# Kernel tuning notes

Measured on AMD Instinct MI355X. Metric: run time of the kernel, lower is better.

The kernel has to match this reference:

```python
import jax, jax.numpy as jnp
import numpy as np

SCALING_FACTOR = 128.0


def setup_inputs() -> dict:
    key = jax.random.key(0)
    k1, k2, k3, k4 = jax.random.split(key, 4)
    B, G1, G2, DX, DZ, NT = 4, 128, 128, 2, 128, 2048
    x_grid = jax.random.uniform(k1, (B, G1, G2, DX), dtype=jnp.float32)
    z_grid = jax.random.normal(k2, (B, G1, G2, DZ), dtype=jnp.float32)
    xt = jax.random.uniform(k3, (B, NT, DX), dtype=jnp.float32)
    # raw (pre-softplus) lengthscale parameter, one per input dim
    init_ls = 0.1
    lengthscale_param = jnp.full((DX,), np.log(np.exp(init_ls) - 1.0), dtype=jnp.float32)
    lengthscale_param = lengthscale_param + 0.01 * jax.random.normal(k4, (DX,), dtype=jnp.float32)
    return {"x_grid": x_grid, "z_grid": z_grid, "xt": xt, "lengthscale_param": lengthscale_param}


def reference(x_grid, z_grid, xt, lengthscale_param):
    B = x_grid.shape[0]
    dx = x_grid.shape[-1]
    dz = z_grid.shape[-1]
    # flatten spatial grid dims -> (B, ng, d)
    xg = x_grid.reshape(B, -1, dx)
    zg = z_grid.reshape(B, -1, dz)
    # lengthscale = 1e-5 + softplus(param), shape (dx,)
    ls = 1e-5 + jax.nn.softplus(lengthscale_param)
    # pairwise scaled squared distances: (B, nt, ng)
    diff = (xt[:, :, None, :] - xg[:, None, :, :]) / ls  # (B, nt, ng, dx)
    dist2 = jnp.sum(diff * diff, axis=-1)
    weights = jnp.exp(-0.5 * dist2)  # (B, nt, ng)
    # weighted smoothing onto targets
    out = jnp.einsum("btg,bgz->btz", weights, zg) / SCALING_FACTOR
    return out
```

## Files before the change

### kernel.cpp

```cpp
#include <hip/hip_runtime.h>
#include <hip/hip_bf16.h>
#include <cstdint>
#include <cstddef>


typedef float  f32x4  __attribute__((ext_vector_type(4)));
typedef float  f32x16 __attribute__((ext_vector_type(16)));
typedef short  short8 __attribute__((ext_vector_type(8)));
typedef unsigned short ushort8 __attribute__((ext_vector_type(8)));

#if __has_builtin(__builtin_amdgcn_exp2f)
#define EXP2F(x) __builtin_amdgcn_exp2f(x)
#else
#define EXP2F(x) exp2f(x)
#endif

#define AS1C(p) ((const __attribute__((address_space(1))) void*)(p))
#define AS3(p)  ((__attribute__((address_space(3))) void*)(p))

__device__ __forceinline__ unsigned short bf16_bits(float f) {
  __bf16 h = (__bf16)f;
  return __builtin_bit_cast(unsigned short, h);
}

__global__ __launch_bounds__(256) void pre_kernel(
    const float* __restrict__ x_grid, const float* __restrict__ z_grid,
    const float* __restrict__ xt, const float* __restrict__ lsp,
    unsigned short* __restrict__ zgb, float* __restrict__ xg_trip,
    float* __restrict__ xt_trip)
{
  const int bid = blockIdx.x;
  const int b   = bid >> 9;
  const int t   = bid & 511;
  const int tid = threadIdx.x;

  const size_t zbase = (size_t)b * 16384 * 128;
  unsigned short* dst_tile = zgb + ((size_t)(b * 512 + t)) * 4096;

  #pragma unroll
  for (int it = 0; it < 2; ++it) {
    const int o8 = it * 256 + tid;
    const int h  = o8 >> 8;
    const int q2 = (o8 >> 7) & 1;
    const int c  = o8 & 127;
    const int kb = t * 32 + h * 16 + q2 * 4;
    ushort8 v;
    #pragma unroll
    for (int hi = 0; hi < 2; ++hi)
      #pragma unroll
      for (int j = 0; j < 4; ++j) {
        float f = z_grid[zbase + (size_t)(kb + 8 * hi + j) * 128 + c];
        v[hi * 4 + j] = bf16_bits(f);
      }
    *(ushort8*)(dst_tile + o8 * 8) = v;
  }

  if (tid < 64) {
    const float ls0 = 1e-5f + log1pf(expf(lsp[0]));
    const float ls1 = 1e-5f + log1pf(expf(lsp[1]));
    const float cs  = sqrtf(0.7213475204444817f);
    const float s0 = cs / ls0, s1 = cs / ls1;
    if (tid < 32) {
      const int g = t * 32 + tid;
      const float u0 = x_grid[(size_t)(b * 16384 + g) * 2 + 0] * s0;
      const float u1 = x_grid[(size_t)(b * 16384 + g) * 2 + 1] * s1;
      float* d = xg_trip + (size_t)(b * 512 + t) * 96 + tid * 3;
      d[0] = 2.0f * u0; d[1] = 2.0f * u1; d[2] = -(u0 * u0 + u1 * u1);
    } else if (t < 64) {
      const int r = t * 32 + (tid - 32);
      const float u0 = xt[(size_t)(b * 2048 + r) * 2 + 0] * s0;
      const float u1 = xt[(size_t)(b * 2048 + r) * 2 + 1] * s1;
      float* d = xt_trip + (size_t)(b * 2048 + r) * 3;
      d[0] = u0; d[1] = u1; d[2] = -(u0 * u0 + u1 * u1);
    }
  }
}

__global__ __launch_bounds__(512, 2) void main_kernel(
    const unsigned short* __restrict__ zgb,
    const float* __restrict__ xg_trip,
    const float* __restrict__ xt_trip,
    float* __restrict__ partials)
{
  __shared__ __align__(128) char smem[24576];
  char*  zbuf  = smem;
  float* xgbuf = (float*)(smem + 16384);

  const int bid = blockIdx.x;
  const int ks  = bid & 3;
  const int mt  = (bid >> 2) & 15;
  const int b   = bid >> 6;

  const int tid = threadIdx.x;
  const int wv  = tid >> 6;
  const int l   = tid & 63;
  const int rh  = wv & 1;
  const int kp  = wv >> 1;
  const int h   = kp & 1;
  const int tp  = kp >> 1;
  const int l31 = l & 31;
  const int q2  = l >> 5;

  float at0[2], at1[2], ca[2];
  #pragma unroll
  for (int mi = 0; mi < 2; ++mi) {
    const int r = mt * 128 + rh * 64 + mi * 32 + l31;
    const float* p = xt_trip + (size_t)(b * 2048 + r) * 3;
    at0[mi] = p[0]; at1[mi] = p[1]; ca[mi] = p[2];
  }

  f32x16 acc[2][4];
  #pragma unroll
  for (int mi = 0; mi < 2; ++mi)
    #pragma unroll
    for (int ni = 0; ni < 4; ++ni)
      #pragma unroll
      for (int e = 0; e < 16; ++e)
        acc[mi][ni][e] = 0.0f;

  const size_t tilebase = (size_t)(b * 512 + ks * 128);
  const char*  zsrc = (const char*)zgb + tilebase * 8192;
  const char*  xsrc = (const char*)(xg_trip) + tilebase * 384;

  auto stage = [&](int t, int bb) {
    __builtin_amdgcn_global_load_lds(
        AS1C(zsrc + (size_t)t * 8192 + wv * 1024 + l * 16),
        AS3(zbuf + bb * 8192 + wv * 1024 + l * 16), 16, 0, 0);
    if (l < 3) {
      __builtin_amdgcn_global_load_lds(
          AS1C(xsrc + (size_t)t * 384 + wv * 48 + l * 16),
          AS3((char*)xgbuf + bb * 384 + wv * 48 + l * 16), 16, 0, 0);
    }
  };

  stage(0, 0);

  for (int t = 0; t < 128; ++t) {
    __syncthreads();
    if (t + 1 < 128) stage(t + 1, (t + 1) & 1);
    if ((t & 1) == tp) {
      const int bb = t & 1;

      const f32x4* xq = (const f32x4*)(xgbuf + bb * 96 + (h * 16 + q2 * 4) * 3);
      const f32x4 A0 = xq[0], A1 = xq[1], A2 = xq[2];
      const f32x4 B0 = xq[6], B1 = xq[7], B2 = xq[8];
      float g0[8], g1[8], cb[8];
      g0[0]=A0.x; g1[0]=A0.y; cb[0]=A0.z;
      g0[1]=A0.w; g1[1]=A1.x; cb[1]=A1.y;
      g0[2]=A1.z; g1[2]=A1.w; cb[2]=A2.x;
      g0[3]=A2.y; g1[3]=A2.z; cb[3]=A2.w;
      g0[4]=B0.x; g1[4]=B0.y; cb[4]=B0.z;
      g0[5]=B0.w; g1[5]=B1.x; cb[5]=B1.y;
      g0[6]=B1.z; g1[6]=B1.w; cb[6]=B2.x;
      g0[7]=B2.y; g1[7]=B2.z; cb[7]=B2.w;

      short8 af[2];
      #pragma unroll
      for (int mi = 0; mi < 2; ++mi) {
        union { short8 s; __bf16 e[8]; } u;
        #pragma unroll
        for (int j = 0; j < 8; ++j) {
          float arg = __builtin_fmaf(at0[mi], g0[j],
                      __builtin_fmaf(at1[mi], g1[j], ca[mi] + cb[j]));
          u.e[j] = (__bf16)EXP2F(arg);
        }
        af[mi] = u.s;
      }

      const char* zt = zbuf + bb * 8192 + h * 4096 + (q2 * 128 + l31) * 16;
      short8 bfr[4];
      #pragma unroll
      for (int ni = 0; ni < 4; ++ni)
        bfr[ni] = *(const short8*)(zt + ni * 512);

      #pragma unroll
      for (int mi = 0; mi < 2; ++mi)
        #pragma unroll
        for (int ni = 0; ni < 4; ++ni)
          acc[mi][ni] = __builtin_amdgcn_mfma_f32_32x32x16_bf16(
              af[mi], bfr[ni], acc[mi][ni], 0, 0, 0);
    }
  }

  __syncthreads();
  float* red = (float*)smem;
  float* pb = partials + ((size_t)(ks * 64 + b * 16 + mt)) * 16384;

  #pragma unroll
  for (int mi = 0; mi < 2; ++mi)
    #pragma unroll
    for (int ni = 0; ni < 4; ++ni) {
      if (kp != 0)
        *(f32x16*)(red + ((rh * 3 + (kp - 1)) * 64 + l) * 16) = acc[mi][ni];
      __syncthreads();
      if (kp == 0) {
        f32x16 s = acc[mi][ni];
        #pragma unroll
        for (int src = 0; src < 3; ++src) {
          const f32x4* sp = (const f32x4*)(red + ((rh * 3 + src) * 64 + l) * 16);
          #pragma unroll
          for (int q = 0; q < 4; ++q) {
            f32x4 v = sp[q];
            s[q*4+0] += v.x; s[q*4+1] += v.y; s[q*4+2] += v.z; s[q*4+3] += v.w;
          }
        }
        const int colb = ni * 32 + l31;
        const int rowb = rh * 64 + mi * 32 + 4 * q2;
        #pragma unroll
        for (int r = 0; r < 16; ++r) {
          const int row = rowb + (r & 3) + 8 * (r >> 2);
          pb[row * 128 + colb] = s[r];
        }
      }
      __syncthreads();
    }
}

__global__ __launch_bounds__(256) void reduce_kernel(
    const float* __restrict__ partials, float* __restrict__ out)
{
  const size_t base = ((size_t)blockIdx.x * 256 + threadIdx.x) * 4;
  const int b  = (int)(base >> 18);
  const int mt = (int)(base >> 14) & 15;
  const int rc = (int)(base & 16383);
  const float* p = partials + ((size_t)(b * 16 + mt)) * 16384 + rc;
  f32x4 s = *(const f32x4*)p;
  #pragma unroll
  for (int ksv = 1; ksv < 4; ++ksv) {
    f32x4 v = *(const f32x4*)(p + (size_t)ksv * 64 * 16384);
    s.x += v.x; s.y += v.y; s.z += v.z; s.w += v.w;
  }
  const float inv = 1.0f / 128.0f;
  s.x *= inv; s.y *= inv; s.z *= inv; s.w *= inv;
  *(f32x4*)(out + base) = s;
}

extern "C" void kernel_launch(void* const* d_in, const int* in_sizes, int n_in,
                              void* d_out, int out_size, void* d_ws, size_t ws_size,
                              hipStream_t stream) {
  const float* x_grid = (const float*)d_in[0];
  const float* z_grid = (const float*)d_in[1];
  const float* xt     = (const float*)d_in[2];
  const float* lsp    = (const float*)d_in[3];
  float* out = (float*)d_out;

  char* ws = (char*)d_ws;
  unsigned short* zgb = (unsigned short*)ws;
  float* xg_trip  = (float*)(ws + 16777216);
  float* xt_trip  = (float*)(ws + 16777216 + 786432);
  float* partials = (float*)(ws + 16777216 + 786432 + 98304);

  pre_kernel<<<2048, 256, 0, stream>>>(x_grid, z_grid, xt, lsp,
                                       zgb, xg_trip, xt_trip);
  main_kernel<<<256, 512, 0, stream>>>(zgb, xg_trip, xt_trip, partials);
  reduce_kernel<<<1024, 256, 0, stream>>>(partials, out);
}
```

Before: 159.9 us.

## Triple-buffer main loop, use all waves per step, atomic output reduction

The main loop is restructured so that all eight waves do MFMA work on every step: each wave owns a k-quarter of a 64-step loop, instead of half the waves idling on alternate steps. Staging now uses a three-buffer LDS ring with explicit vmcnt waits, so loads run two stages ahead. The 1/128 scale is folded into the bf16 conversion of z in the pre-kernel. The partials buffer and the reduce kernel are replaced by a memset plus float atomicAdd into the output. In exchange, this adds atomic traffic and nondeterministic summation order, and uses more LDS per block.

```diff
diff --git a/kernel.cpp b/kernel.cpp
--- a/kernel.cpp
+++ b/kernel.cpp
@@ -18,41 +18,36 @@
 #define AS1C(p) ((const __attribute__((address_space(1))) void*)(p))
 #define AS3(p)  ((__attribute__((address_space(3))) void*)(p))
 
-__device__ __forceinline__ unsigned short bf16_bits(float f) {
-  __bf16 h = (__bf16)f;
-  return __builtin_bit_cast(unsigned short, h);
-}
-
 __global__ __launch_bounds__(256) void pre_kernel(
     const float* __restrict__ x_grid, const float* __restrict__ z_grid,
     const float* __restrict__ xt, const float* __restrict__ lsp,
     unsigned short* __restrict__ zgb, float* __restrict__ xg_trip,
-    float* __restrict__ xt_trip)
+    float* __restrict__ xt4)
 {
   const int bid = blockIdx.x;
   const int b   = bid >> 9;
   const int t   = bid & 511;
   const int tid = threadIdx.x;
+  const int q2  = tid >> 7;
+  const int c   = tid & 127;
 
   const size_t zbase = (size_t)b * 16384 * 128;
-  unsigned short* dst_tile = zgb + ((size_t)(b * 512 + t)) * 4096;
-
-  #pragma unroll
-  for (int it = 0; it < 2; ++it) {
-    const int o8 = it * 256 + tid;
-    const int h  = o8 >> 8;
-    const int q2 = (o8 >> 7) & 1;
-    const int c  = o8 & 127;
+  const float  sc = 1.0f / 128.0f;
+
+  #pragma unroll
+  for (int h = 0; h < 2; ++h) {
     const int kb = t * 32 + h * 16 + q2 * 4;
     ushort8 v;
     #pragma unroll
     for (int hi = 0; hi < 2; ++hi)
       #pragma unroll
       for (int j = 0; j < 4; ++j) {
-        float f = z_grid[zbase + (size_t)(kb + 8 * hi + j) * 128 + c];
-        v[hi * 4 + j] = bf16_bits(f);
-      }
-    *(ushort8*)(dst_tile + o8 * 8) = v;
+        float f = z_grid[zbase + (size_t)(kb + 8 * hi + j) * 128 + c] * sc;
+        __bf16 hb = (__bf16)f;
+        v[hi * 4 + j] = __builtin_bit_cast(unsigned short, hb);
+      }
+    *(ushort8*)(zgb + ((size_t)(b * 1024 + 2 * t + h)) * 2048
+                    + (size_t)(q2 * 128 + c) * 8) = v;
   }
 
   if (tid < 64) {
@@ -62,29 +57,31 @@
     const float s0 = cs / ls0, s1 = cs / ls1;
     if (tid < 32) {
       const int g = t * 32 + tid;
-      const float u0 = x_grid[(size_t)(b * 16384 + g) * 2 + 0] * s0;
-      const float u1 = x_grid[(size_t)(b * 16384 + g) * 2 + 1] * s1;
-      float* d = xg_trip + (size_t)(b * 512 + t) * 96 + tid * 3;
+      const float u0 = x_grid[((size_t)(b * 16384 + g)) * 2 + 0] * s0;
+      const float u1 = x_grid[((size_t)(b * 16384 + g)) * 2 + 1] * s1;
+      float* d = xg_trip + ((size_t)(b * 16384 + g)) * 3;
       d[0] = 2.0f * u0; d[1] = 2.0f * u1; d[2] = -(u0 * u0 + u1 * u1);
     } else if (t < 64) {
       const int r = t * 32 + (tid - 32);
-      const float u0 = xt[(size_t)(b * 2048 + r) * 2 + 0] * s0;
-      const float u1 = xt[(size_t)(b * 2048 + r) * 2 + 1] * s1;
-      float* d = xt_trip + (size_t)(b * 2048 + r) * 3;
-      d[0] = u0; d[1] = u1; d[2] = -(u0 * u0 + u1 * u1);
+      const float u0 = xt[((size_t)(b * 2048 + r)) * 2 + 0] * s0;
+      const float u1 = xt[((size_t)(b * 2048 + r)) * 2 + 1] * s1;
+      f32x4 d; d.x = u0; d.y = u1; d.z = -(u0 * u0 + u1 * u1); d.w = 0.0f;
+      *(f32x4*)(xt4 + ((size_t)(b * 2048 + r)) * 4) = d;
     }
   }
 }
+
+#define BUFSTRIDE 17408
+#define ZOFF(buf, kq) ((buf) * BUFSTRIDE + (kq) * 4096)
+#define TOFF(buf, kq) ((buf) * BUFSTRIDE + 16384 + (kq) * 256)
 
 __global__ __launch_bounds__(512, 2) void main_kernel(
     const unsigned short* __restrict__ zgb,
     const float* __restrict__ xg_trip,
-    const float* __restrict__ xt_trip,
-    float* __restrict__ partials)
+    const float* __restrict__ xt4,
+    float* __restrict__ out)
 {
-  __shared__ __align__(128) char smem[24576];
-  char*  zbuf  = smem;
-  float* xgbuf = (float*)(smem + 16384);
+  __shared__ __align__(128) char smem[3 * BUFSTRIDE];
 
   const int bid = blockIdx.x;
   const int ks  = bid & 3;
@@ -94,10 +91,8 @@
   const int tid = threadIdx.x;
   const int wv  = tid >> 6;
   const int l   = tid & 63;
-  const int rh  = wv & 1;
-  const int kp  = wv >> 1;
-  const int h   = kp & 1;
-  const int tp  = kp >> 1;
+  const int kq  = wv & 3;
+  const int rh  = wv >> 2;
   const int l31 = l & 31;
   const int q2  = l >> 5;
 
@@ -105,8 +100,8 @@
   #pragma unroll
   for (int mi = 0; mi < 2; ++mi) {
     const int r = mt * 128 + rh * 64 + mi * 32 + l31;
-    const float* p = xt_trip + (size_t)(b * 2048 + r) * 3;
-    at0[mi] = p[0]; at1[mi] = p[1]; ca[mi] = p[2];
+    f32x4 v = *(const f32x4*)(xt4 + ((size_t)(b * 2048 + r)) * 4);
+    at0[mi] = v.x; at1[mi] = v.y; ca[mi] = v.z;
   }
 
   f32x16 acc[2][4];
@@ -118,121 +113,144 @@
       for (int e = 0; e < 16; ++e)
         acc[mi][ni][e] = 0.0f;
 
-  const size_t tilebase = (size_t)(b * 512 + ks * 128);
-  const char*  zsrc = (const char*)zgb + tilebase * 8192;
-  const char*  xsrc = (const char*)(xg_trip) + tilebase * 384;
-
-  auto stage = [&](int t, int bb) {
-    __builtin_amdgcn_global_load_lds(
-        AS1C(zsrc + (size_t)t * 8192 + wv * 1024 + l * 16),
-        AS3(zbuf + bb * 8192 + wv * 1024 + l * 16), 16, 0, 0);
-    if (l < 3) {
-      __builtin_amdgcn_global_load_lds(
-          AS1C(xsrc + (size_t)t * 384 + wv * 48 + l * 16),
-          AS3((char*)xgbuf + bb * 384 + wv * 48 + l * 16), 16, 0, 0);
+  const char* zsrc0 = (const char*)zgb
+                    + ((size_t)(b * 1024 + ks * 256 + kq * 64)) * 4096;
+  const char* tsrc0 = (const char*)xg_trip
+                    + ((size_t)(b * 1024 + ks * 256 + kq * 64)) * 192;
+
+  auto stage = [&](int s) {
+    const int buf = s % 3;
+    const char* zs = zsrc0 + (size_t)s * 4096;
+    char* zd = smem + ZOFF(buf, kq);
+    __builtin_amdgcn_global_load_lds(AS1C(zs + rh * 2048 + l * 16),
+                                     AS3(zd + rh * 2048 + l * 16), 16, 0, 0);
+    __builtin_amdgcn_global_load_lds(AS1C(zs + rh * 2048 + 1024 + l * 16),
+                                     AS3(zd + rh * 2048 + 1024 + l * 16), 16, 0, 0);
+    if (l < 6) {
+      const char* ts = tsrc0 + (size_t)s * 192 + rh * 96;
+      char* td = smem + TOFF(buf, kq) + rh * 96;
+      __builtin_amdgcn_global_load_lds(AS1C(ts + l * 16),
+                                       AS3(td + l * 16), 16, 0, 0);
     }
   };
 
-  stage(0, 0);
-
-  for (int t = 0; t < 128; ++t) {
-    __syncthreads();
-    if (t + 1 < 128) stage(t + 1, (t + 1) & 1);
-    if ((t & 1) == tp) {
-      const int bb = t & 1;
-
-      const f32x4* xq = (const f32x4*)(xgbuf + bb * 96 + (h * 16 + q2 * 4) * 3);
-      const f32x4 A0 = xq[0], A1 = xq[1], A2 = xq[2];
-      const f32x4 B0 = xq[6], B1 = xq[7], B2 = xq[8];
-      float g0[8], g1[8], cb[8];
-      g0[0]=A0.x; g1[0]=A0.y; cb[0]=A0.z;
-      g0[1]=A0.w; g1[1]=A1.x; cb[1]=A1.y;
-      g0[2]=A1.z; g1[2]=A1.w; cb[2]=A2.x;
-      g0[3]=A2.y; g1[3]=A2.z; cb[3]=A2.w;
-      g0[4]=B0.x; g1[4]=B0.y; cb[4]=B0.z;
-      g0[5]=B0.w; g1[5]=B1.x; cb[5]=B1.y;
-      g0[6]=B1.z; g1[6]=B1.w; cb[6]=B2.x;
-      g0[7]=B2.y; g1[7]=B2.z; cb[7]=B2.w;
-
-      short8 af[2];
-      #pragma unroll
-      for (int mi = 0; mi < 2; ++mi) {
-        union { short8 s; __bf16 e[8]; } u;
-        #pragma unroll
-        for (int j = 0; j < 8; ++j) {
-          float arg = __builtin_fmaf(at0[mi], g0[j],
-                      __builtin_fmaf(at1[mi], g1[j], ca[mi] + cb[j]));
-          u.e[j] = (__bf16)EXP2F(arg);
-        }
-        af[mi] = u.s;
-      }
-
-      const char* zt = zbuf + bb * 8192 + h * 4096 + (q2 * 128 + l31) * 16;
-      short8 bfr[4];
+  stage(0);
+  stage(1);
+
+  #pragma unroll 3
+  for (int s = 0; s < 64; ++s) {
+    if (s < 63) { asm volatile("s_waitcnt vmcnt(3)" ::: "memory"); }
+    else        { asm volatile("s_waitcnt vmcnt(0)" ::: "memory"); }
+    __builtin_amdgcn_s_barrier();
+    asm volatile("" ::: "memory");
+
+    if (s + 2 < 64) stage(s + 2);
+
+    const int buf = s % 3;
+
+    const float* tb = (const float*)(smem + TOFF(buf, kq) + q2 * 48);
+    union { f32x4 v[3]; float f[12]; } lo, hi;
+    lo.v[0] = *(const f32x4*)(tb + 0);
+    lo.v[1] = *(const f32x4*)(tb + 4);
+    lo.v[2] = *(const f32x4*)(tb + 8);
+    hi.v[0] = *(const f32x4*)(tb + 24);
+    hi.v[1] = *(const f32x4*)(tb + 28);
+    hi.v[2] = *(const f32x4*)(tb + 32);
+
+    const char* zt = smem + ZOFF(buf, kq) + q2 * 2048 + l31 * 16;
+    short8 bfr[4];
+    #pragma unroll
+    for (int ni = 0; ni < 4; ++ni)
+      bfr[ni] = *(const short8*)(zt + ni * 512);
+
+    short8 af[2];
+    #pragma unroll
+    for (int mi = 0; mi < 2; ++mi) {
+      union { short8 s8; __bf16 e[8]; } u;
+      #pragma unroll
+      for (int j = 0; j < 4; ++j) {
+        float arg = __builtin_fmaf(at0[mi], lo.f[3 * j],
+                    __builtin_fmaf(at1[mi], lo.f[3 * j + 1],
+                                   ca[mi] + lo.f[3 * j + 2]));
+        u.e[j] = (__bf16)EXP2F(arg);
+      }
+      #pragma unroll
+      for (int j = 0; j < 4; ++j) {
+        float arg = __builtin_fmaf(at0[mi], hi.f[3 * j],
+                    __builtin_fmaf(at1[mi], hi.f[3 * j + 1],
+                                   ca[mi] + hi.f[3 * j + 2]));
+        u.e[4 + j] = (__bf16)EXP2F(arg);
+      }
+      af[mi] = u.s8;
+    }
+
+    #pragma unroll
+    for (int mi = 0; mi < 2; ++mi)
       #pragma unroll
       for (int ni = 0; ni < 4; ++ni)
-        bfr[ni] = *(const short8*)(zt + ni * 512);
-
-      #pragma unroll
-      for (int mi = 0; mi < 2; ++mi)
-        #pragma unroll
-        for (int ni = 0; ni < 4; ++ni)
-          acc[mi][ni] = __builtin_amdgcn_mfma_f32_32x32x16_bf16(
-              af[mi], bfr[ni], acc[mi][ni], 0, 0, 0);
-    }
+        acc[mi][ni] = __builtin_amdgcn_mfma_f32_32x32x16_bf16(
+            af[mi], bfr[ni], acc[mi][ni], 0, 0, 0);
   }
 
   __syncthreads();
   float* red = (float*)smem;
-  float* pb = partials + ((size_t)(ks * 64 + b * 16 + mt)) * 16384;
-
-  #pragma unroll
-  for (int mi = 0; mi < 2; ++mi)
-    #pragma unroll
-    for (int ni = 0; ni < 4; ++ni) {
-      if (kp != 0)
-        *(f32x16*)(red + ((rh * 3 + (kp - 1)) * 64 + l) * 16) = acc[mi][ni];
-      __syncthreads();
-      if (kp == 0) {
-        f32x16 s = acc[mi][ni];
+
+  #pragma unroll
+  for (int mi = 0; mi < 2; ++mi) {
+    #pragma unroll
+    for (int np = 0; np < 2; ++np) {
+      if (kq != 0) {
+        const int w = rh * 3 + (kq - 1);
         #pragma unroll
-        for (int src = 0; src < 3; ++src) {
-          const f32x4* sp = (const f32x4*)(red + ((rh * 3 + src) * 64 + l) * 16);
+        for (int nj = 0; nj < 2; ++nj) {
+          const int ni = np * 2 + nj;
           #pragma unroll
           for (int q = 0; q < 4; ++q) {
-            f32x4 v = sp[q];
-            s[q*4+0] += v.x; s[q*4+1] += v.y; s[q*4+2] += v.z; s[q*4+3] += v.w;
+            f32x4 qv;
+            qv.x = acc[mi][ni][q * 4 + 0];
+            qv.y = acc[mi][ni][q * 4 + 1];
+            qv.z = acc[mi][ni][q * 4 + 2];
+            qv.w = acc[mi][ni][q * 4 + 3];
+            *(f32x4*)(red + w * 2048 + nj * 1024 + q * 256 + l * 4) = qv;
           }
         }
-        const int colb = ni * 32 + l31;
-        const int rowb = rh * 64 + mi * 32 + 4 * q2;
+      }
+      __syncthreads();
+      if (kq == 0) {
+        #pragma unroll
+        for (int nj = 0; nj < 2; ++nj) {
+          const int ni = np * 2 + nj;
+          #pragma unroll
+          for (int src = 0; src < 3; ++src) {
+            const int w = rh * 3 + src;
+            #pragma unroll
+            for (int q = 0; q < 4; ++q) {
+              f32x4 v = *(const f32x4*)(red + w * 2048 + nj * 1024 + q * 256 + l * 4);
+              acc[mi][ni][q * 4 + 0] += v.x;
+              acc[mi][ni][q * 4 + 1] += v.y;
+              acc[mi][ni][q * 4 + 2] += v.z;
+              acc[mi][ni][q * 4 + 3] += v.w;
+            }
+          }
+        }
+      }
+      __syncthreads();
+    }
+  }
+
+  if (kq == 0) {
+    #pragma unroll
+    for (int mi = 0; mi < 2; ++mi)
+      #pragma unroll
+      for (int ni = 0; ni < 4; ++ni)
         #pragma unroll
         for (int r = 0; r < 16; ++r) {
-          const int row = rowb + (r & 3) + 8 * (r >> 2);
-          pb[row * 128 + colb] = s[r];
+          const int row = mt * 128 + rh * 64 + mi * 32
+                        + (r & 3) + 8 * (r >> 2) + 4 * q2;
+          atomicAdd(out + ((size_t)b * 2048 + row) * 128 + ni * 32 + l31,
+                    acc[mi][ni][r]);
         }
-      }
-      __syncthreads();
-    }
-}
-
-__global__ __launch_bounds__(256) void reduce_kernel(
-    const float* __restrict__ partials, float* __restrict__ out)
-{
-  const size_t base = ((size_t)blockIdx.x * 256 + threadIdx.x) * 4;
-  const int b  = (int)(base >> 18);
-  const int mt = (int)(base >> 14) & 15;
-  const int rc = (int)(base & 16383);
-  const float* p = partials + ((size_t)(b * 16 + mt)) * 16384 + rc;
-  f32x4 s = *(const f32x4*)p;
-  #pragma unroll
-  for (int ksv = 1; ksv < 4; ++ksv) {
-    f32x4 v = *(const f32x4*)(p + (size_t)ksv * 64 * 16384);
-    s.x += v.x; s.y += v.y; s.z += v.z; s.w += v.w;
-  }
-  const float inv = 1.0f / 128.0f;
-  s.x *= inv; s.y *= inv; s.z *= inv; s.w *= inv;
-  *(f32x4*)(out + base) = s;
+  }
 }
 
 extern "C" void kernel_launch(void* const* d_in, const int* in_sizes, int n_in,
@@ -246,12 +264,11 @@
 
   char* ws = (char*)d_ws;
   unsigned short* zgb = (unsigned short*)ws;
-  float* xg_trip  = (float*)(ws + 16777216);
-  float* xt_trip  = (float*)(ws + 16777216 + 786432);
-  float* partials = (float*)(ws + 16777216 + 786432 + 98304);
-
+  float* xg_trip = (float*)(ws + 16777216);
+  float* xt4     = (float*)(ws + 16777216 + 786432);
+
+  hipMemsetAsync(d_out, 0, (size_t)out_size * sizeof(float), stream);
   pre_kernel<<<2048, 256, 0, stream>>>(x_grid, z_grid, xt, lsp,
-                                       zgb, xg_trip, xt_trip);
-  main_kernel<<<256, 512, 0, stream>>>(zgb, xg_trip, xt_trip, partials);
-  reduce_kernel<<<1024, 256, 0, stream>>>(partials, out);
+                                       zgb, xg_trip, xt4);
+  main_kernel<<<256, 512, 0, stream>>>(zgb, xg_trip, xt4, out);
 }
```

Result: faster. 145.4 us (-9.0%).
